# Performance work log

Measured on AMD Instinct MI355X. Metric: run time of the kernel, lower is better.

Reference implementation:

```python
import jax, jax.numpy as jnp
import numpy as np


def _lstm(x, W_ih, W_hh, b_ih, b_hh):
    """PyTorch-convention LSTM. x: [B, T, I] -> (ys [B, T, H], h_T [B, H]).
    Gate order i, f, g, o as in torch.nn.LSTM."""
    def step(carry, xt):
        h, c = carry
        gates = xt @ W_ih.T + b_ih + h @ W_hh.T + b_hh
        i, f, g, o = jnp.split(gates, 4, axis=-1)
        c = jax.nn.sigmoid(f) * c + jax.nn.sigmoid(i) * jnp.tanh(g)
        h = jax.nn.sigmoid(o) * jnp.tanh(c)
        return (h, c), h
    B = x.shape[0]
    H = W_hh.shape[1]
    init = (jnp.zeros((B, H), x.dtype), jnp.zeros((B, H), x.dtype))
    (hT, _), ys = jax.lax.scan(step, init, jnp.swapaxes(x, 0, 1))
    return jnp.swapaxes(ys, 0, 1), hT


def setup_inputs():
    key = jax.random.key(0)
    ks = jax.random.split(key, 13)
    B, S, F = 256, 1024, 16
    p = lambda k, shape: jax.random.normal(k, shape, jnp.float32) * 0.1
    return {
        "x": jax.random.normal(ks[0], (B, S, F), jnp.float32),
        "data": 0,
        "W_ih1": p(ks[1], (32, 1)),  "W_hh1": p(ks[2], (32, 8)),
        "b_ih1": p(ks[3], (32,)),    "b_hh1": p(ks[4], (32,)),
        "W_ih2": p(ks[5], (512, 8)), "W_hh2": p(ks[6], (512, 128)),
        "b_ih2": p(ks[7], (512,)),   "b_hh2": p(ks[8], (512,)),
        "W1": p(ks[9], (64, 128)),   "b1": p(ks[10], (64,)),
        "W2": p(ks[11], (1, 64)),    "b2": p(ks[12], (1,)),
    }


def reference(x, data, W_ih1, W_hh1, b_ih1, b_hh1,
              W_ih2, W_hh2, b_ih2, b_hh2, W1, b1, W2, b2):
    B, S, F = x.shape
    # rnn1: original loops over batch; here all B*S rows are one big batch of
    # length-F sequences with feature dim 1. We only need the final hidden h_T.
    x1 = x.reshape(B * S, F, 1)
    _, h1 = _lstm(x1, W_ih1, W_hh1, b_ih1, b_hh1)            # [B*S, 8]
    # original does .detach().numpy() -> gradient is cut here
    h1 = jax.lax.stop_gradient(h1).reshape(B, S, 8)
    ys2, _ = _lstm(h1, W_ih2, W_hh2, b_ih2, b_hh2)           # [B, S, 128]
    last = ys2[:, -1, :]                                     # [B, 128]
    return (last @ W1.T + b1) @ W2.T + b2                    # [B, 1]
```

## Files before the change

kernel.cpp:

```cpp
#include <hip/hip_runtime.h>
#include <cstdint>

typedef _Float16 f16x2 __attribute__((ext_vector_type(2)));

__device__ __forceinline__ float fsig(float x) {
  return __fdividef(1.f, 1.f + __expf(-x));
}
__device__ __forceinline__ float ftanh_(float x) {
  return fmaf(2.f, fsig(x + x), -1.f);
}
__device__ __forceinline__ int packf16(float a, float b) {
  f16x2 p; p.x = (_Float16)a; p.y = (_Float16)b;
  return __builtin_bit_cast(int, p);
}
__device__ __forceinline__ float dot2(int w, int h, float acc) {
  return __builtin_amdgcn_fdot2(__builtin_bit_cast(f16x2, w),
                                __builtin_bit_cast(f16x2, h), acc, false);
}
template <int CTRL>
__device__ __forceinline__ float qp(float v) {
  return __int_as_float(__builtin_amdgcn_update_dpp(
      0, __float_as_int(v), CTRL, 0xF, 0xF, true));
}
#define QP_X1 0xB1

__global__ __launch_bounds__(256, 2) void lstm1_kernel(
    const float* __restrict__ x, const float* __restrict__ Wih,
    const float* __restrict__ Whh, const float* __restrict__ bih,
    const float* __restrict__ bhh, int4* __restrict__ h1out) {
  const int n = blockIdx.x * 256 + threadIdx.x;

  int whh2[128];
#pragma unroll
  for (int r = 0; r < 32; ++r) {
#pragma unroll
    for (int j = 0; j < 4; ++j) {
      float2 v = ((const float2*)(Whh + r * 8))[j];
      whh2[r * 4 + j] = packf16(v.x, v.y);
    }
  }
  int wxb[32];
#pragma unroll
  for (int r = 0; r < 32; ++r) wxb[r] = packf16(Wih[r], bih[r] + bhh[r]);

#pragma unroll
  for (int i = 0; i < 128; i += 8)
    asm volatile("" : "+v"(whh2[i]), "+v"(whh2[i + 1]), "+v"(whh2[i + 2]),
                      "+v"(whh2[i + 3]), "+v"(whh2[i + 4]), "+v"(whh2[i + 5]),
                      "+v"(whh2[i + 6]), "+v"(whh2[i + 7]));
#pragma unroll
  for (int i = 0; i < 32; i += 8)
    asm volatile("" : "+v"(wxb[i]), "+v"(wxb[i + 1]), "+v"(wxb[i + 2]),
                      "+v"(wxb[i + 3]), "+v"(wxb[i + 4]), "+v"(wxb[i + 5]),
                      "+v"(wxb[i + 6]), "+v"(wxb[i + 7]));

  const float* __restrict__ xp = x + (size_t)n * 16;
  float c[8];
  int h2[4];
#pragma unroll
  for (int k = 0; k < 8; ++k) c[k] = 0.f;
#pragma unroll
  for (int j = 0; j < 4; ++j) h2[j] = 0;

  float xv = xp[0];
#pragma unroll 1
  for (int t = 0; t < 16; ++t) {
    float xn = xp[(t + 1) & 15];
    const int xt1 = packf16(xv, 1.f);
    float hn[8];
#pragma unroll
    for (int k = 0; k < 8; ++k) {
      float acc[4];
#pragma unroll
      for (int gi = 0; gi < 4; ++gi) {
        const int r = gi * 8 + k;
        float a = dot2(wxb[r], xt1, 0.f);
        a = dot2(whh2[r * 4 + 0], h2[0], a);
        a = dot2(whh2[r * 4 + 1], h2[1], a);
        a = dot2(whh2[r * 4 + 2], h2[2], a);
        a = dot2(whh2[r * 4 + 3], h2[3], a);
        acc[gi] = a;
      }
      float iv = fsig(acc[0]), fv = fsig(acc[1]);
      float gv = ftanh_(acc[2]), ov = fsig(acc[3]);
      c[k] = fmaf(fv, c[k], iv * gv);
      hn[k] = ov * ftanh_(c[k]);
    }
#pragma unroll
    for (int j = 0; j < 4; ++j) h2[j] = packf16(hn[2 * j], hn[2 * j + 1]);
    xv = xn;
  }
  int4 o;
  o.x = h2[0]; o.y = h2[1]; o.z = h2[2]; o.w = h2[3];
  h1out[n] = o;
}

__global__ __launch_bounds__(256, 1) void lstm2_kernel(
    const int4* __restrict__ h1, const float* __restrict__ Wih,
    const float* __restrict__ Whh, const float* __restrict__ bih,
    const float* __restrict__ bhh, const float* __restrict__ Wd1,
    const float* __restrict__ bd1, const float* __restrict__ Wd2,
    const float* __restrict__ bd2, float* __restrict__ out) {
  __shared__ __align__(16) _Float16 sH[2][128];
  const int b = blockIdx.x;
  const int t = threadIdx.x;
  const int m = t >> 1;
  const int q = t & 1;
  const bool isq1 = (q == 1);

  int w[128];
#pragma unroll
  for (int g = 0; g < 4; ++g) {
    const float2* p = (const float2*)(Whh + (size_t)(g * 128 + m) * 128 + q * 64);
#pragma unroll
    for (int j = 0; j < 32; ++j) {
      float2 v = p[j];
      w[g * 32 + j] = packf16(v.x, v.y);
    }
  }
#pragma unroll
  for (int i = 0; i < 128; i += 8)
    asm volatile("" : "+v"(w[i]), "+v"(w[i + 1]), "+v"(w[i + 2]),
                      "+v"(w[i + 3]), "+v"(w[i + 4]), "+v"(w[i + 5]),
                      "+v"(w[i + 6]), "+v"(w[i + 7]));

  int wigA[4], wigB[4];
  float biasA, biasB;
  {
    const int rowA = (2 * q) * 128 + m;
    const int rowB = (2 * q + 1) * 128 + m;
    const float2* pa = (const float2*)(Wih + (size_t)rowA * 8);
    const float2* pb = (const float2*)(Wih + (size_t)rowB * 8);
#pragma unroll
    for (int j = 0; j < 4; ++j) {
      float2 va = pa[j], vb = pb[j];
      wigA[j] = packf16(va.x, va.y);
      wigB[j] = packf16(vb.x, vb.y);
    }
    biasA = bih[rowA] + bhh[rowA];
    biasB = bih[rowB] + bhh[rowB];
  }

  int hq[32];
#pragma unroll
  for (int i = 0; i < 32; ++i) hq[i] = 0;
  float c = 0.f;

  const int4* __restrict__ xg = h1 + (size_t)b * 1024;
  int4 xc = xg[0];
  int4 xn = xg[1];

#pragma unroll 1
  for (int ts = 0; ts < 1024; ++ts) {
    float bxA = biasA, bxB = biasB;
    bxA = dot2(wigA[0], xc.x, bxA);
    bxA = dot2(wigA[1], xc.y, bxA);
    bxA = dot2(wigA[2], xc.z, bxA);
    bxA = dot2(wigA[3], xc.w, bxA);
    bxB = dot2(wigB[0], xc.x, bxB);
    bxB = dot2(wigB[1], xc.y, bxB);
    bxB = dot2(wigB[2], xc.z, bxB);
    bxB = dot2(wigB[3], xc.w, bxB);

    float R0a = 0.f, R1a = 0.f, R2a = 0.f, R3a = 0.f;
    float R0b = 0.f, R1b = 0.f, R2b = 0.f, R3b = 0.f;
#pragma unroll
    for (int j = 0; j < 16; ++j) {
      R0a = dot2(w[j], hq[j], R0a);
      R1a = dot2(w[32 + j], hq[j], R1a);
      R2a = dot2(w[64 + j], hq[j], R2a);
      R3a = dot2(w[96 + j], hq[j], R3a);
    }
#pragma unroll
    for (int j = 16; j < 32; ++j) {
      R0b = dot2(w[j], hq[j], R0b);
      R1b = dot2(w[32 + j], hq[j], R1b);
      R2b = dot2(w[64 + j], hq[j], R2b);
      R3b = dot2(w[96 + j], hq[j], R3b);
    }
    float R0 = R0a + R0b, R1 = R1a + R1b;
    float R2 = R2a + R2b, R3 = R3a + R3b;

    float vA = isq1 ? R0 : R2;
    float Sa = (isq1 ? R2 : R0) + qp<QP_X1>(vA) + bxA;
    float vB = isq1 ? R1 : R3;
    float Sb = (isq1 ? R3 : R1) + qp<QP_X1>(vB) + bxB;

    float ua = isq1 ? (Sa + Sa) : Sa;
    float sga = fsig(ua);
    float actA = isq1 ? fmaf(2.f, sga, -1.f) : sga;
    float actB = fsig(Sb);

    float ga = qp<QP_X1>(actA);
    float gb = qp<QP_X1>(actB);
    float iv = isq1 ? ga : actA;
    float gv = isq1 ? actA : ga;
    float fv = isq1 ? gb : actB;
    float ov = isq1 ? actB : gb;

    c = fmaf(fv, c, iv * gv);
    float hx = ov * ftanh_(c);
    if (!isq1) sH[ts & 1][m] = (_Float16)hx;
    __syncthreads();

    {
      const int4* src = (const int4*)(&sH[ts & 1][q * 64]);
      int4 A = src[0], B = src[1], C = src[2], D = src[3];
      int4 E = src[4], F = src[5], G2 = src[6], H = src[7];
      hq[0] = A.x;   hq[1] = A.y;   hq[2] = A.z;   hq[3] = A.w;
      hq[4] = B.x;   hq[5] = B.y;   hq[6] = B.z;   hq[7] = B.w;
      hq[8] = C.x;   hq[9] = C.y;   hq[10] = C.z;  hq[11] = C.w;
      hq[12] = D.x;  hq[13] = D.y;  hq[14] = D.z;  hq[15] = D.w;
      hq[16] = E.x;  hq[17] = E.y;  hq[18] = E.z;  hq[19] = E.w;
      hq[20] = F.x;  hq[21] = F.y;  hq[22] = F.z;  hq[23] = F.w;
      hq[24] = G2.x; hq[25] = G2.y; hq[26] = G2.z; hq[27] = G2.w;
      hq[28] = H.x;  hq[29] = H.y;  hq[30] = H.z;  hq[31] = H.w;
      xc = xn;
      xn = xg[ts < 1022 ? ts + 2 : 1023];
    }
  }

  if (t < 64) {
    float a = bd1[t];
#pragma unroll
    for (int k = 0; k < 128; ++k)
      a = fmaf(Wd1[t * 128 + k], (float)sH[1][k], a);
    float v = a * Wd2[t];
#pragma unroll
    for (int off = 32; off > 0; off >>= 1) v += __shfl_down(v, off);
    if (t == 0) out[b] = v + bd2[0];
  }
}

extern "C" void kernel_launch(void* const* d_in, const int* in_sizes, int n_in,
                              void* d_out, int out_size, void* d_ws, size_t ws_size,
                              hipStream_t stream) {
  const float* x    = (const float*)d_in[0];
  const float* Wih1 = (const float*)d_in[2];
  const float* Whh1 = (const float*)d_in[3];
  const float* bih1 = (const float*)d_in[4];
  const float* bhh1 = (const float*)d_in[5];
  const float* Wih2 = (const float*)d_in[6];
  const float* Whh2 = (const float*)d_in[7];
  const float* bih2 = (const float*)d_in[8];
  const float* bhh2 = (const float*)d_in[9];
  const float* W1   = (const float*)d_in[10];
  const float* b1   = (const float*)d_in[11];
  const float* W2   = (const float*)d_in[12];
  const float* b2   = (const float*)d_in[13];
  float* out = (float*)d_out;

  int4* h1 = (int4*)d_ws;

  lstm1_kernel<<<1024, 256, 0, stream>>>(x, Wih1, Whh1, bih1, bhh1, h1);
  lstm2_kernel<<<256, 256, 0, stream>>>(h1, Wih2, Whh2, bih2, bhh2,
                                        W1, b1, W2, b2, out);
}
```

Measured before the change: 786.4 us.

## Fuse LSTM1 into LSTM2 kernel via shared memory and prescale log2e into weights

Merges the two kernels into one. Each block first computes the 1024 layer-1 hidden states for its batch row into LDS, then runs the layer-2 recurrence reading inputs from LDS, which removes the global round trip and the second launch. Gate weights and biases are prescaled by log2(e) (doubled for the g gate) so the activations use exp2 and a hardware reciprocal. The layer-2 loop is unrolled by two with constant LDS buffer indices. In exchange, layer 1 now runs on only 256 blocks at occupancy 1, where it previously used 1024 blocks at occupancy 2, so its phase may take longer.

```diff
diff --git a/kernel.cpp b/kernel.cpp
--- a/kernel.cpp
+++ b/kernel.cpp
@@ -3,11 +3,13 @@
 
 typedef _Float16 f16x2 __attribute__((ext_vector_type(2)));
 
-__device__ __forceinline__ float fsig(float x) {
-  return __fdividef(1.f, 1.f + __expf(-x));
-}
-__device__ __forceinline__ float ftanh_(float x) {
-  return fmaf(2.f, fsig(x + x), -1.f);
+#define L2E 1.44269504f
+
+__device__ __forceinline__ float sig2(float y) {
+  return __builtin_amdgcn_rcpf(1.f + exp2f(-y));
+}
+__device__ __forceinline__ float tanhc(float c) {
+  return fmaf(2.f, __builtin_amdgcn_rcpf(1.f + exp2f(c * (-2.f * L2E))), -1.f);
 }
 __device__ __forceinline__ int packf16(float a, float b) {
   f16x2 p; p.x = (_Float16)a; p.y = (_Float16)b;
@@ -24,86 +26,88 @@
 }
 #define QP_X1 0xB1
 
-__global__ __launch_bounds__(256, 2) void lstm1_kernel(
-    const float* __restrict__ x, const float* __restrict__ Wih,
-    const float* __restrict__ Whh, const float* __restrict__ bih,
-    const float* __restrict__ bhh, int4* __restrict__ h1out) {
-  const int n = blockIdx.x * 256 + threadIdx.x;
-
-  int whh2[128];
-#pragma unroll
-  for (int r = 0; r < 32; ++r) {
-#pragma unroll
-    for (int j = 0; j < 4; ++j) {
-      float2 v = ((const float2*)(Whh + r * 8))[j];
-      whh2[r * 4 + j] = packf16(v.x, v.y);
-    }
-  }
-  int wxb[32];
-#pragma unroll
-  for (int r = 0; r < 32; ++r) wxb[r] = packf16(Wih[r], bih[r] + bhh[r]);
-
-#pragma unroll
-  for (int i = 0; i < 128; i += 8)
-    asm volatile("" : "+v"(whh2[i]), "+v"(whh2[i + 1]), "+v"(whh2[i + 2]),
-                      "+v"(whh2[i + 3]), "+v"(whh2[i + 4]), "+v"(whh2[i + 5]),
-                      "+v"(whh2[i + 6]), "+v"(whh2[i + 7]));
-#pragma unroll
-  for (int i = 0; i < 32; i += 8)
-    asm volatile("" : "+v"(wxb[i]), "+v"(wxb[i + 1]), "+v"(wxb[i + 2]),
-                      "+v"(wxb[i + 3]), "+v"(wxb[i + 4]), "+v"(wxb[i + 5]),
-                      "+v"(wxb[i + 6]), "+v"(wxb[i + 7]));
-
-  const float* __restrict__ xp = x + (size_t)n * 16;
-  float c[8];
-  int h2[4];
-#pragma unroll
-  for (int k = 0; k < 8; ++k) c[k] = 0.f;
-#pragma unroll
-  for (int j = 0; j < 4; ++j) h2[j] = 0;
-
-  float xv = xp[0];
-#pragma unroll 1
-  for (int t = 0; t < 16; ++t) {
-    float xn = xp[(t + 1) & 15];
-    const int xt1 = packf16(xv, 1.f);
-    float hn[8];
-#pragma unroll
-    for (int k = 0; k < 8; ++k) {
-      float acc[4];
-#pragma unroll
-      for (int gi = 0; gi < 4; ++gi) {
-        const int r = gi * 8 + k;
-        float a = dot2(wxb[r], xt1, 0.f);
-        a = dot2(whh2[r * 4 + 0], h2[0], a);
-        a = dot2(whh2[r * 4 + 1], h2[1], a);
-        a = dot2(whh2[r * 4 + 2], h2[2], a);
-        a = dot2(whh2[r * 4 + 3], h2[3], a);
-        acc[gi] = a;
-      }
-      float iv = fsig(acc[0]), fv = fsig(acc[1]);
-      float gv = ftanh_(acc[2]), ov = fsig(acc[3]);
-      c[k] = fmaf(fv, c[k], iv * gv);
-      hn[k] = ov * ftanh_(c[k]);
-    }
-#pragma unroll
-    for (int j = 0; j < 4; ++j) h2[j] = packf16(hn[2 * j], hn[2 * j + 1]);
-    xv = xn;
-  }
-  int4 o;
-  o.x = h2[0]; o.y = h2[1]; o.z = h2[2]; o.w = h2[3];
-  h1out[n] = o;
-}
-
-__global__ __launch_bounds__(256, 1) void lstm2_kernel(
-    const int4* __restrict__ h1, const float* __restrict__ Wih,
-    const float* __restrict__ Whh, const float* __restrict__ bih,
-    const float* __restrict__ bhh, const float* __restrict__ Wd1,
+__global__ __launch_bounds__(256, 1) void fused_kernel(
+    const float* __restrict__ x, const float* __restrict__ Wih1,
+    const float* __restrict__ Whh1, const float* __restrict__ bih1,
+    const float* __restrict__ bhh1, const float* __restrict__ Wih2,
+    const float* __restrict__ Whh2, const float* __restrict__ bih2,
+    const float* __restrict__ bhh2, const float* __restrict__ Wd1,
     const float* __restrict__ bd1, const float* __restrict__ Wd2,
     const float* __restrict__ bd2, float* __restrict__ out) {
+  __shared__ __align__(16) int4 sX[1026];
   __shared__ __align__(16) _Float16 sH[2][128];
+
   const int b = blockIdx.x;
   const int t = threadIdx.x;
+
+  {
+    int whh2[128];
+#pragma unroll
+    for (int r = 0; r < 32; ++r) {
+      const float s = (r >> 3) == 2 ? 2.f * L2E : L2E;
+#pragma unroll
+      for (int j = 0; j < 4; ++j) {
+        float2 v = ((const float2*)(Whh1 + r * 8))[j];
+        whh2[r * 4 + j] = packf16(v.x * s, v.y * s);
+      }
+    }
+    int wxb[32];
+#pragma unroll
+    for (int r = 0; r < 32; ++r) {
+      const float s = (r >> 3) == 2 ? 2.f * L2E : L2E;
+      wxb[r] = packf16(Wih1[r] * s, (bih1[r] + bhh1[r]) * s);
+    }
+#pragma unroll
+    for (int i = 0; i < 128; i += 8)
+      asm volatile("" : "+v"(whh2[i]), "+v"(whh2[i + 1]), "+v"(whh2[i + 2]),
+                        "+v"(whh2[i + 3]), "+v"(whh2[i + 4]), "+v"(whh2[i + 5]),
+                        "+v"(whh2[i + 6]), "+v"(whh2[i + 7]));
+
+#pragma unroll 1
+    for (int ch = 0; ch < 4; ++ch) {
+      const int c = ch * 256 + t;
+      const float* __restrict__ xp = x + ((size_t)b * 1024 + c) * 16;
+      float cc[8];
+      int h2[4];
+#pragma unroll
+      for (int k = 0; k < 8; ++k) cc[k] = 0.f;
+#pragma unroll
+      for (int j = 0; j < 4; ++j) h2[j] = 0;
+
+      float xv = xp[0];
+#pragma unroll 1
+      for (int u = 0; u < 16; ++u) {
+        float xnl = xp[(u + 1) & 15];
+        const int xt1 = packf16(xv, 1.f);
+        float hn[8];
+#pragma unroll
+        for (int k = 0; k < 8; ++k) {
+          float acc[4];
+#pragma unroll
+          for (int gi = 0; gi < 4; ++gi) {
+            const int r = gi * 8 + k;
+            float a = dot2(wxb[r], xt1, 0.f);
+            a = dot2(whh2[r * 4 + 0], h2[0], a);
+            a = dot2(whh2[r * 4 + 1], h2[1], a);
+            a = dot2(whh2[r * 4 + 2], h2[2], a);
+            a = dot2(whh2[r * 4 + 3], h2[3], a);
+            acc[gi] = a;
+          }
+          float iv = sig2(acc[0]), fv = sig2(acc[1]);
+          float gv = fmaf(2.f, sig2(acc[2]), -1.f), ov = sig2(acc[3]);
+          cc[k] = fmaf(fv, cc[k], iv * gv);
+          hn[k] = ov * tanhc(cc[k]);
+        }
+#pragma unroll
+        for (int j = 0; j < 4; ++j) h2[j] = packf16(hn[2 * j], hn[2 * j + 1]);
+        xv = xnl;
+      }
+      int4 o;
+      o.x = h2[0]; o.y = h2[1]; o.z = h2[2]; o.w = h2[3];
+      sX[c] = o;
+    }
+  }
+
   const int m = t >> 1;
   const int q = t & 1;
   const bool isq1 = (q == 1);
@@ -111,11 +115,12 @@
   int w[128];
 #pragma unroll
   for (int g = 0; g < 4; ++g) {
-    const float2* p = (const float2*)(Whh + (size_t)(g * 128 + m) * 128 + q * 64);
+    const float s = (g == 2) ? 2.f * L2E : L2E;
+    const float2* p = (const float2*)(Whh2 + (size_t)(g * 128 + m) * 128 + q * 64);
 #pragma unroll
     for (int j = 0; j < 32; ++j) {
       float2 v = p[j];
-      w[g * 32 + j] = packf16(v.x, v.y);
+      w[g * 32 + j] = packf16(v.x * s, v.y * s);
     }
   }
 #pragma unroll
@@ -127,18 +132,21 @@
   int wigA[4], wigB[4];
   float biasA, biasB;
   {
-    const int rowA = (2 * q) * 128 + m;
-    const int rowB = (2 * q + 1) * 128 + m;
-    const float2* pa = (const float2*)(Wih + (size_t)rowA * 8);
-    const float2* pb = (const float2*)(Wih + (size_t)rowB * 8);
+    const int gA = 2 * q, gB = 2 * q + 1;
+    const float sa = (gA == 2) ? 2.f * L2E : L2E;
+    const float sb = L2E;
+    const int rowA = gA * 128 + m;
+    const int rowB = gB * 128 + m;
+    const float2* pa = (const float2*)(Wih2 + (size_t)rowA * 8);
+    const float2* pb = (const float2*)(Wih2 + (size_t)rowB * 8);
 #pragma unroll
     for (int j = 0; j < 4; ++j) {
       float2 va = pa[j], vb = pb[j];
-      wigA[j] = packf16(va.x, va.y);
-      wigB[j] = packf16(vb.x, vb.y);
-    }
-    biasA = bih[rowA] + bhh[rowA];
-    biasB = bih[rowB] + bhh[rowB];
+      wigA[j] = packf16(va.x * sa, va.y * sa);
+      wigB[j] = packf16(vb.x * sb, vb.y * sb);
+    }
+    biasA = (bih2[rowA] + bhh2[rowA]) * sa;
+    biasB = (bih2[rowB] + bhh2[rowB]) * sb;
   }
 
   int hq[32];
@@ -146,79 +154,75 @@
   for (int i = 0; i < 32; ++i) hq[i] = 0;
   float c = 0.f;
 
-  const int4* __restrict__ xg = h1 + (size_t)b * 1024;
-  int4 xc = xg[0];
-  int4 xn = xg[1];
+  __syncthreads();
+  int4 xc = sX[0];
+
+#define LSTM2_STEP(BUF, NEXT_IDX)                                          \
+  {                                                                        \
+    float bxA = biasA, bxB = biasB;                                        \
+    bxA = dot2(wigA[0], xc.x, bxA);                                        \
+    bxA = dot2(wigA[1], xc.y, bxA);                                        \
+    bxA = dot2(wigA[2], xc.z, bxA);                                        \
+    bxA = dot2(wigA[3], xc.w, bxA);                                        \
+    bxB = dot2(wigB[0], xc.x, bxB);                                        \
+    bxB = dot2(wigB[1], xc.y, bxB);                                        \
+    bxB = dot2(wigB[2], xc.z, bxB);                                        \
+    bxB = dot2(wigB[3], xc.w, bxB);                                        \
+    float R0a = 0.f, R1a = 0.f, R2a = 0.f, R3a = 0.f;                      \
+    float R0b = 0.f, R1b = 0.f, R2b = 0.f, R3b = 0.f;                      \
+    _Pragma("unroll")                                                      \
+    for (int j = 0; j < 16; ++j) {                                         \
+      R0a = dot2(w[j], hq[j], R0a);                                        \
+      R1a = dot2(w[32 + j], hq[j], R1a);                                   \
+      R2a = dot2(w[64 + j], hq[j], R2a);                                   \
+      R3a = dot2(w[96 + j], hq[j], R3a);                                   \
+    }                                                                      \
+    _Pragma("unroll")                                                      \
+    for (int j = 16; j < 32; ++j) {                                        \
+      R0b = dot2(w[j], hq[j], R0b);                                        \
+      R1b = dot2(w[32 + j], hq[j], R1b);                                   \
+      R2b = dot2(w[64 + j], hq[j], R2b);                                   \
+      R3b = dot2(w[96 + j], hq[j], R3b);                                   \
+    }                                                                      \
+    float R0 = R0a + R0b, R1 = R1a + R1b;                                  \
+    float R2 = R2a + R2b, R3 = R3a + R3b;                                  \
+    float vA = isq1 ? R0 : R2;                                             \
+    float Sa = (isq1 ? R2 : R0) + qp<QP_X1>(vA) + bxA;                     \
+    float vB = isq1 ? R1 : R3;                                             \
+    float Sb = (isq1 ? R3 : R1) + qp<QP_X1>(vB) + bxB;                     \
+    float sga = sig2(Sa);                                                  \
+    float actA = isq1 ? fmaf(2.f, sga, -1.f) : sga;                        \
+    float actB = sig2(Sb);                                                 \
+    float ga = qp<QP_X1>(actA);                                            \
+    float gb = qp<QP_X1>(actB);                                            \
+    float iv = isq1 ? ga : actA;                                           \
+    float gv = isq1 ? actA : ga;                                           \
+    float fv = isq1 ? gb : actB;                                           \
+    float ov = isq1 ? actB : gb;                                           \
+    c = fmaf(fv, c, iv * gv);                                              \
+    float hx = ov * tanhc(c);                                              \
+    if (!isq1) sH[BUF][m] = (_Float16)hx;                                  \
+    __syncthreads();                                                       \
+    const int4* src = (const int4*)(&sH[BUF][q * 64]);                     \
+    int4 A = src[0], Bv = src[1], C = src[2], D = src[3];                  \
+    int4 E = src[4], F = src[5], G2 = src[6], H = src[7];                  \
+    hq[0] = A.x;   hq[1] = A.y;   hq[2] = A.z;   hq[3] = A.w;              \
+    hq[4] = Bv.x;  hq[5] = Bv.y;  hq[6] = Bv.z;  hq[7] = Bv.w;             \
+    hq[8] = C.x;   hq[9] = C.y;   hq[10] = C.z;  hq[11] = C.w;             \
+    hq[12] = D.x;  hq[13] = D.y;  hq[14] = D.z;  hq[15] = D.w;             \
+    hq[16] = E.x;  hq[17] = E.y;  hq[18] = E.z;  hq[19] = E.w;             \
+    hq[20] = F.x;  hq[21] = F.y;  hq[22] = F.z;  hq[23] = F.w;             \
+    hq[24] = G2.x; hq[25] = G2.y; hq[26] = G2.z; hq[27] = G2.w;            \
+    hq[28] = H.x;  hq[29] = H.y;  hq[30] = H.z;  hq[31] = H.w;             \
+    xc = sX[NEXT_IDX];                                                     \
+  }
 
 #pragma unroll 1
-  for (int ts = 0; ts < 1024; ++ts) {
-    float bxA = biasA, bxB = biasB;
-    bxA = dot2(wigA[0], xc.x, bxA);
-    bxA = dot2(wigA[1], xc.y, bxA);
-    bxA = dot2(wigA[2], xc.z, bxA);
-    bxA = dot2(wigA[3], xc.w, bxA);
-    bxB = dot2(wigB[0], xc.x, bxB);
-    bxB = dot2(wigB[1], xc.y, bxB);
-    bxB = dot2(wigB[2], xc.z, bxB);
-    bxB = dot2(wigB[3], xc.w, bxB);
-
-    float R0a = 0.f, R1a = 0.f, R2a = 0.f, R3a = 0.f;
-    float R0b = 0.f, R1b = 0.f, R2b = 0.f, R3b = 0.f;
-#pragma unroll
-    for (int j = 0; j < 16; ++j) {
-      R0a = dot2(w[j], hq[j], R0a);
-      R1a = dot2(w[32 + j], hq[j], R1a);
-      R2a = dot2(w[64 + j], hq[j], R2a);
-      R3a = dot2(w[96 + j], hq[j], R3a);
-    }
-#pragma unroll
-    for (int j = 16; j < 32; ++j) {
-      R0b = dot2(w[j], hq[j], R0b);
-      R1b = dot2(w[32 + j], hq[j], R1b);
-      R2b = dot2(w[64 + j], hq[j], R2b);
-      R3b = dot2(w[96 + j], hq[j], R3b);
-    }
-    float R0 = R0a + R0b, R1 = R1a + R1b;
-    float R2 = R2a + R2b, R3 = R3a + R3b;
-
-    float vA = isq1 ? R0 : R2;
-    float Sa = (isq1 ? R2 : R0) + qp<QP_X1>(vA) + bxA;
-    float vB = isq1 ? R1 : R3;
-    float Sb = (isq1 ? R3 : R1) + qp<QP_X1>(vB) + bxB;
-
-    float ua = isq1 ? (Sa + Sa) : Sa;
-    float sga = fsig(ua);
-    float actA = isq1 ? fmaf(2.f, sga, -1.f) : sga;
-    float actB = fsig(Sb);
-
-    float ga = qp<QP_X1>(actA);
-    float gb = qp<QP_X1>(actB);
-    float iv = isq1 ? ga : actA;
-    float gv = isq1 ? actA : ga;
-    float fv = isq1 ? gb : actB;
-    float ov = isq1 ? actB : gb;
-
-    c = fmaf(fv, c, iv * gv);
-    float hx = ov * ftanh_(c);
-    if (!isq1) sH[ts & 1][m] = (_Float16)hx;
-    __syncthreads();
-
-    {
-      const int4* src = (const int4*)(&sH[ts & 1][q * 64]);
-      int4 A = src[0], B = src[1], C = src[2], D = src[3];
-      int4 E = src[4], F = src[5], G2 = src[6], H = src[7];
-      hq[0] = A.x;   hq[1] = A.y;   hq[2] = A.z;   hq[3] = A.w;
-      hq[4] = B.x;   hq[5] = B.y;   hq[6] = B.z;   hq[7] = B.w;
-      hq[8] = C.x;   hq[9] = C.y;   hq[10] = C.z;  hq[11] = C.w;
-      hq[12] = D.x;  hq[13] = D.y;  hq[14] = D.z;  hq[15] = D.w;
-      hq[16] = E.x;  hq[17] = E.y;  hq[18] = E.z;  hq[19] = E.w;
-      hq[20] = F.x;  hq[21] = F.y;  hq[22] = F.z;  hq[23] = F.w;
-      hq[24] = G2.x; hq[25] = G2.y; hq[26] = G2.z; hq[27] = G2.w;
-      hq[28] = H.x;  hq[29] = H.y;  hq[30] = H.z;  hq[31] = H.w;
-      xc = xn;
-      xn = xg[ts < 1022 ? ts + 2 : 1023];
-    }
-  }
+  for (int ts2 = 0; ts2 < 512; ++ts2) {
+    LSTM2_STEP(0, 2 * ts2 + 1)
+    LSTM2_STEP(1, 2 * ts2 + 2)
+  }
+#undef LSTM2_STEP
 
   if (t < 64) {
     float a = bd1[t];
@@ -250,9 +254,7 @@
   const float* b2   = (const float*)d_in[13];
   float* out = (float*)d_out;
 
-  int4* h1 = (int4*)d_ws;
-
-  lstm1_kernel<<<1024, 256, 0, stream>>>(x, Wih1, Whh1, bih1, bhh1, h1);
-  lstm2_kernel<<<256, 256, 0, stream>>>(h1, Wih2, Whh2, bih2, bhh2,
+  fused_kernel<<<256, 256, 0, stream>>>(x, Wih1, Whh1, bih1, bhh1,
+                                        Wih2, Whh2, bih2, bhh2,
                                         W1, b1, W2, b2, out);
 }
```

Measured after the change: 659.3 us. -16.2%, faster.
